# Kernel tuning notes

Measured on AMD Instinct MI355X. Metric: run time of the kernel, lower is better.

Reference implementation:

```python
import jax, jax.numpy as jnp
import numpy as np

N, E, H = 25000, 100000, 32          # nodes, edges, node/clique hidden dim
NC, A, EC = 8000, 50000, 24000       # cliques, node2clique assignments, clique edges
EEMB, CEE, L = 8, 8, 2               # edge emb dims, n layers


def segment_mean(vals, ids, num):
    s = jax.ops.segment_sum(vals, ids, num_segments=num)
    cnt = jax.ops.segment_sum(jnp.ones(ids.shape[0], vals.dtype), ids, num_segments=num)
    return s / jnp.maximum(cnt, 1.0)[:, None]


def setup_inputs() -> dict:
    key = jax.random.key(0)
    ks = jax.random.split(key, 24)
    s = 0.1  # param scale
    inp = {
        "node_features": jax.random.normal(ks[0], (N, H), jnp.float32),
        "edge_index": jax.random.randint(ks[1], (2, E), 0, N),
        "edge_features": jax.random.normal(ks[2], (E, EEMB), jnp.float32),
        "clique_features": jax.random.normal(ks[3], (NC, H), jnp.float32),
        "node2clique_index": jnp.stack([
            jax.random.randint(ks[4], (A,), 0, N),
            jax.random.randint(ks[5], (A,), 0, NC)]),
        "clique_edge_index": jax.random.randint(ks[6], (2, EC), 0, NC),
        "clique_edge_features": jax.random.normal(ks[7], (EC, CEE), jnp.float32),
        # node NNConv params (stacked over L layers)
        "nn1_w": jax.random.normal(ks[8], (L, EEMB, H)) * s,
        "nn1_b": jnp.zeros((L, H)),
        "nn2_w": jax.random.normal(ks[9], (L, H, H * H)) * s,
        "nn2_b": jnp.zeros((L, H * H)),
        "root_w": jax.random.normal(ks[10], (L, H, H)) * s,
        "root_b": jnp.zeros((L, H)),
        # Node2Clique linear
        "n2c_w": jax.random.normal(ks[11], (L, H, H)) * s,
        "n2c_b": jnp.zeros((L, H)),
        # clique NNConv params
        "cnn1_w": jax.random.normal(ks[12], (L, CEE, H)) * s,
        "cnn1_b": jnp.zeros((L, H)),
        "cnn2_w": jax.random.normal(ks[13], (L, H, H * H)) * s,
        "cnn2_b": jnp.zeros((L, H * H)),
        "croot_w": jax.random.normal(ks[14], (L, H, H)) * s,
        "croot_b": jnp.zeros((L, H)),
        # Clique2Node linear
        "c2n_w": jax.random.normal(ks[15], (L, H, H)) * s,
        "c2n_b": jnp.zeros((L, H)),
    }
    return inp


def nnconv(x, src, dst, edge_attr, w1, b1, w2, b2, rw, rb, n_out_nodes):
    # per-edge weight matrices from the edge MLP: [E, in, out]
    h = jax.nn.relu(edge_attr @ w1 + b1)
    We = (h @ w2 + b2).reshape(edge_attr.shape[0], x.shape[1], -1)
    msg = jnp.einsum('ei,eio->eo', x[src], We)           # message from source
    agg = segment_mean(msg, dst, n_out_nodes)            # mean aggregation at target
    return agg + x @ rw + rb                             # root weight + bias


def reference(node_features, edge_index, edge_features, clique_features,
              node2clique_index, clique_edge_index, clique_edge_features,
              nn1_w, nn1_b, nn2_w, nn2_b, root_w, root_b, n2c_w, n2c_b,
              cnn1_w, cnn1_b, cnn2_w, cnn2_b, croot_w, croot_b, c2n_w, c2n_b):
    x, c = node_features, clique_features
    src, dst = edge_index[0], edge_index[1]
    nid, cid = node2clique_index[0], node2clique_index[1]
    csrc, cdst = clique_edge_index[0], clique_edge_index[1]
    for l in range(L):
        # node-level edge-conditioned conv
        x = jax.nn.relu(nnconv(x, src, dst, edge_features,
                               nn1_w[l], nn1_b[l], nn2_w[l], nn2_b[l],
                               root_w[l], root_b[l], N))
        # Node2Clique: project node feats, scatter-mean into cliques
        m = x @ n2c_w[l] + n2c_b[l]
        c = c + segment_mean(m[nid], cid, NC)
        # clique-level edge-conditioned conv
        c = jax.nn.relu(nnconv(c, csrc, cdst, clique_edge_features,
                               cnn1_w[l], cnn1_b[l], cnn2_w[l], cnn2_b[l],
                               croot_w[l], croot_b[l], NC))
        # Clique2Node: project clique feats, scatter-mean back onto nodes
        m = c @ c2n_w[l] + c2n_b[l]
        x = x + segment_mean(m[cid], nid, N)
    return (x, c)
```

## Files before the change

kernel.cpp:

```cpp
#include <hip/hip_runtime.h>
#include <hip/hip_bf16.h>

typedef unsigned int u32;
typedef unsigned short u16;

#define DEVINL __device__ __forceinline__

constexpr int Nn  = 25000;
constexpr int Ee  = 100000;
constexpr int NCc = 8000;
constexpr int Aa  = 50000;
constexpr int ECc = 24000;
constexpr int TCOLS = 1088;
constexpr int WPSZ  = TCOLS*32;
constexpr int TT_ROW = 561;
constexpr int NB_N = (Nn + 255)/256;
constexpr int NB_C = (NCc + 255)/256;
constexpr int PB_EN = (Ee + 255)/256;
constexpr int PB_EC = (ECc + 255)/256;
constexpr int PB_AS = (2*Aa + 255)/256;
constexpr int PB_WP = (4*WPSZ + 255)/256;

typedef float f32x4 __attribute__((ext_vector_type(4)));
typedef _Float16 h16x2 __attribute__((ext_vector_type(2)));
typedef _Float16 h16x8 __attribute__((ext_vector_type(8)));

DEVINL float b2f(u16 u){ union{u32 i;float f;}v; v.i = ((u32)u)<<16; return v.f; }
DEVINL float bfl(u32 u){ union{u32 i;float f;}v; v.i = u<<16; return v.f; }
DEVINL float bfh(u32 u){ union{u32 i;float f;}v; v.i = u & 0xffff0000u; return v.f; }
DEVINL u16 f2b(float f){ union{float f;u32 i;}v; v.f=f; u32 i=v.i;
  return (u16)((i + 0x7fffu + ((i>>16)&1u)) >> 16); }
DEVINL u16 f2h(float x){ union{ _Float16 h; u16 u; } v; v.h = (_Float16)x; return v.u; }
DEVINL u32 pkh2(float a, float b){
  union{ _Float16 h[2]; u32 u; } v;
  v.h[0] = (_Float16)a; v.h[1] = (_Float16)b; return v.u;
}
DEVINL float ldw(const void* p, long i, int f){
  return f ? ((const float*)p)[i] : b2f(((const u16*)p)[i]);
}
DEVINL float dot2f(u32 a, u32 b, float c){
  union U{u32 u; h16x2 h;};
  U ua; ua.u = a; U ub; ub.u = b;
#if __has_builtin(__builtin_amdgcn_fdot2)
  return __builtin_amdgcn_fdot2(ua.h, ub.h, c, false);
#else
  return c + (float)ua.h[0]*(float)ub.h[0] + (float)ua.h[1]*(float)ub.h[1];
#endif
}

__global__ __launch_bounds__(256) void k_detect_count(const u16* __restrict__ p, int n,
                        u32* __restrict__ maxbits, int* __restrict__ zcnt,
                        int* __restrict__ done, int* __restrict__ flag,
                        const int* __restrict__ ei, const int* __restrict__ cei,
                        const int* __restrict__ n2c,
                        int* __restrict__ deg_nd, int* __restrict__ deg_ce,
                        int* __restrict__ deg_n2c, int* __restrict__ deg_c2n,
                        int* __restrict__ cnt_sn, int* __restrict__ cnt_sc){
  int i0 = blockIdx.x*256 + threadIdx.x;
  { int t = i0;
    if (t < Ee)                             atomicAdd(&deg_nd[ei[Ee + t]], 1);
    else if ((t -= Ee) < ECc)               atomicAdd(&deg_ce[cei[ECc + t]], 1);
    else if ((t -= ECc) < Aa)               atomicAdd(&deg_n2c[n2c[Aa + t]], 1);
    else if ((t -= Aa) < Aa)                atomicAdd(&deg_c2n[n2c[t]], 1);
    else if ((t -= Aa) < Ee)                atomicAdd(&cnt_sn[ei[t]], 1);
    else if ((t -= Ee) < ECc)               atomicAdd(&cnt_sc[cei[t]], 1);
  }
  if (blockIdx.x >= 256) return;
  float lm = 0.f; int lz = 0;
  for (int i = i0; i < n; i += 256*256){
    u16 v = p[i];
    if (v == 0) lz++;
    lm = fmaxf(lm, fabsf(b2f(v)));
  }
  #pragma unroll
  for (int off = 32; off; off >>= 1){
    lm = fmaxf(lm, __shfl_down(lm, off));
    lz += __shfl_down(lz, off);
  }
  __shared__ float smax[4]; __shared__ int szc[4];
  if ((threadIdx.x & 63) == 0){
    smax[threadIdx.x >> 6] = lm;
    szc[threadIdx.x >> 6] = lz;
  }
  __syncthreads();
  if (threadIdx.x == 0){
    float m = fmaxf(fmaxf(smax[0], smax[1]), fmaxf(smax[2], smax[3]));
    int z = szc[0] + szc[1] + szc[2] + szc[3];
    atomicMax(maxbits, __float_as_uint(m));
    atomicAdd(zcnt, z);
    __threadfence();
    if (atomicAdd(done, 1) == 255){
      float mm = __uint_as_float(*maxbits);
      *flag = (mm > 1e6f || *zcnt > n/4) ? 1 : 0;
    }
  }
}

__global__ __launch_bounds__(256) void k_scan_block(
    const int* __restrict__ c0, const int* __restrict__ c1,
    const int* __restrict__ c2, const int* __restrict__ c3,
    int* __restrict__ o0, int* __restrict__ o1, int* __restrict__ o2, int* __restrict__ o3,
    int* __restrict__ b0, int* __restrict__ b1, int* __restrict__ b2, int* __restrict__ b3){
  __shared__ int s[256];
  int bid = blockIdx.x, seg, rb;
  if (bid < NB_N){ seg=0; rb=bid; }
  else if (bid < NB_N+NB_C){ seg=1; rb=bid-NB_N; }
  else if (bid < 2*NB_N+NB_C){ seg=2; rb=bid-NB_N-NB_C; }
  else { seg=3; rb=bid-2*NB_N-NB_C; }
  const int* cnt = seg==0?c0 : seg==1?c1 : seg==2?c2 : c3;
  int* offs = seg==0?o0 : seg==1?o1 : seg==2?o2 : o3;
  int* bs   = seg==0?b0 : seg==1?b1 : seg==2?b2 : b3;
  int M = (seg & 1) ? NCc : Nn;
  int tid = threadIdx.x;
  int i = rb*256 + tid;
  int v = (i < M) ? cnt[i] : 0;
  s[tid] = v; __syncthreads();
  for (int d = 1; d < 256; d <<= 1){
    int t = (tid >= d) ? s[tid-d] : 0;
    __syncthreads();
    s[tid] += t;
    __syncthreads();
  }
  if (i < M) offs[i] = s[tid] - v;
  if (tid == 255) bs[rb] = s[255];
}

__global__ __launch_bounds__(256) void k_scan_fix2(
    int* __restrict__ o0, int* __restrict__ o1, int* __restrict__ o2, int* __restrict__ o3,
    const int* __restrict__ b0, const int* __restrict__ b1,
    const int* __restrict__ b2, const int* __restrict__ b3){
  __shared__ int s[256];
  int bid = blockIdx.x, seg, rb;
  if (bid < NB_N){ seg=0; rb=bid; }
  else if (bid < NB_N+NB_C){ seg=1; rb=bid-NB_N; }
  else if (bid < 2*NB_N+NB_C){ seg=2; rb=bid-NB_N-NB_C; }
  else { seg=3; rb=bid-2*NB_N-NB_C; }
  int* offs = seg==0?o0 : seg==1?o1 : seg==2?o2 : o3;
  const int* bsp = seg==0?b0 : seg==1?b1 : seg==2?b2 : b3;
  int M = (seg & 1) ? NCc : Nn;
  int tid = threadIdx.x;
  int v = (tid < rb) ? bsp[tid] : 0;
  s[tid] = v; __syncthreads();
  #pragma unroll
  for (int d = 128; d; d >>= 1){
    if (tid < d) s[tid] += s[tid + d];
    __syncthreads();
  }
  int prefix = s[0];
  int i = rb*256 + tid;
  if (i < M) offs[i] += prefix;
}

__global__ __launch_bounds__(256) void k_place_pack(
    const int* __restrict__ ei, const int* __restrict__ cei, const int* __restrict__ n2c,
    const void* __restrict__ ef, const void* __restrict__ cef,
    const void* __restrict__ nn1w, const void* __restrict__ nn1b,
    const void* __restrict__ cnn1w, const void* __restrict__ cnn1b,
    const void* __restrict__ nn2w, const void* __restrict__ nn2b, const void* __restrict__ rootw,
    const void* __restrict__ cnn2w, const void* __restrict__ cnn2b, const void* __restrict__ crootw,
    const int* __restrict__ offs_n, const int* __restrict__ offs_c,
    const int* __restrict__ offs_an, const int* __restrict__ offs_ac,
    int* __restrict__ cur_n, int* __restrict__ cur_c,
    int* __restrict__ cur_an, int* __restrict__ cur_ac,
    int2* __restrict__ sdp_n, int2* __restrict__ sdp_c,
    u32* __restrict__ hp_n, u32* __restrict__ hp_c,
    int* __restrict__ an2c, int* __restrict__ ac2n,
    const int* __restrict__ flag, u16* __restrict__ Wp4){
  int b = blockIdx.x, tid = threadIdx.x;
  int f = *flag;
  if (b < PB_EN + PB_EC){
    __shared__ float w1s[2][256], b1s[2][32];
    int isC = (b >= PB_EN);
    int e = (isC ? b - PB_EN : b)*256 + tid;
    int E = isC ? ECc : Ee;
    const void* W1 = isC ? cnn1w : nn1w;
    const void* B1 = isC ? cnn1b : nn1b;
    w1s[0][tid] = ldw(W1, tid, f);
    w1s[1][tid] = ldw(W1, 256 + tid, f);
    if (tid < 32){ b1s[0][tid] = ldw(B1, tid, f); b1s[1][tid] = ldw(B1, 32 + tid, f); }
    __syncthreads();
    if (e < E){
      const int* EI = isC ? cei : ei;
      int s = EI[e], d = EI[E + e];
      int* cur = isC ? cur_c : cur_n;
      const int* offs = isC ? offs_c : offs_n;
      int p = offs[s] + atomicAdd(&cur[s], 1);
      (isC ? sdp_c : sdp_n)[p] = make_int2(s, d);
      const void* EF = isC ? cef : ef;
      float ev[8];
      #pragma unroll
      for (int j = 0; j < 8; j++) ev[j] = ldw(EF, (long)e*8 + j, f);
      u32* hp = isC ? hp_c : hp_n;
      #pragma unroll
      for (int l = 0; l < 2; l++){
        u32* hq = hp + (size_t)l*E*16 + (size_t)p*16;
        #pragma unroll
        for (int kk = 0; kk < 16; kk++){
          float a0 = b1s[l][2*kk], a1 = b1s[l][2*kk+1];
          #pragma unroll
          for (int j = 0; j < 8; j++){
            a0 += ev[j]*w1s[l][j*32 + 2*kk];
            a1 += ev[j]*w1s[l][j*32 + 2*kk + 1];
          }
          hq[kk] = pkh2(fmaxf(a0, 0.f), fmaxf(a1, 0.f));
        }
      }
    }
  } else if (b < PB_EN + PB_EC + PB_AS){
    int i = (b - PB_EN - PB_EC)*256 + tid;
    if (i < Aa){
      int c = n2c[Aa + i];
      an2c[offs_ac[c] + atomicAdd(&cur_ac[c], 1)] = n2c[i];
    } else if ((i -= Aa) < Aa){
      int nd = n2c[i];
      ac2n[offs_an[nd] + atomicAdd(&cur_an[nd], 1)] = n2c[Aa + i];
    }
  } else {
    int i = (b - PB_EN - PB_EC - PB_AS)*256 + tid;
    if (i >= 4*WPSZ) return;
    int set = i / WPSZ, j = i - set*WPSZ;
    int l = set >> 1, isC = set & 1;
    const void* W2 = isC ? cnn2w : nn2w;
    const void* B2 = isC ? cnn2b : nn2b;
    const void* RW = isC ? crootw : rootw;
    int col = j >> 5, ii = j & 31;
    float v;
    if (col < 1024)      v = ldw(W2, (long)l*32768 + ((col>>5)<<10) + (ii<<5) + (col&31), f);
    else if (col < 1056) v = ldw(B2, (long)l*1024 + (ii<<5) + (col-1024), f);
    else                 v = ldw(RW, (long)l*1024 + (ii<<5) + (col-1056), f);
    Wp4[i] = f2h(v);
  }
}

__global__ __launch_bounds__(512) void k_conv_fused(const void* __restrict__ base, int braw,
                           const float* __restrict__ addagg, const int* __restrict__ adddeg, int M,
                           const int2* __restrict__ sdp, const u32* __restrict__ hp,
                           const int* __restrict__ offs, int E_,
                           const u16* __restrict__ Wp,
                           const void* __restrict__ rb, long rboff,
                           const int* __restrict__ flag,
                           float* __restrict__ feat_root, float* __restrict__ agg){
  __shared__ __align__(16) u32 Tt[16*TT_ROW];
  __shared__ u32 hws[8][64];
  int tid = threadIdx.x;
  int w = tid >> 6, lane = tid & 63;
  int quad = lane >> 4, lm = lane & 15;
  int n0 = blockIdx.x * 16;
  int f = *flag;
  int n = n0 + lm;
  int nc = n < M ? n : M-1;
  long bidx = (long)nc*32 + quad*8;
  float fv[8];
  if (braw && f == 0){
    uint4 q = *(const uint4*)((const u16*)base + bidx);
    fv[0]=bfl(q.x); fv[1]=bfh(q.x); fv[2]=bfl(q.y); fv[3]=bfh(q.y);
    fv[4]=bfl(q.z); fv[5]=bfh(q.z); fv[6]=bfl(q.w); fv[7]=bfh(q.w);
  } else {
    const float4* bp = (const float4*)((const float*)base + bidx);
    float4 q0 = bp[0], q1 = bp[1];
    fv[0]=q0.x; fv[1]=q0.y; fv[2]=q0.z; fv[3]=q0.w;
    fv[4]=q1.x; fv[5]=q1.y; fv[6]=q1.z; fv[7]=q1.w;
  }
  if (addagg){
    int dg = adddeg[nc];
    float d = (float)(dg > 1 ? dg : 1);
    const float4* ap = (const float4*)(addagg + (size_t)nc*32 + quad*8);
    float4 a0 = ap[0], a1 = ap[1];
    float inv = 1.f/d;
    fv[0]+=a0.x*inv; fv[1]+=a0.y*inv; fv[2]+=a0.z*inv; fv[3]+=a0.w*inv;
    fv[4]+=a1.x*inv; fv[5]+=a1.y*inv; fv[6]+=a1.z*inv; fv[7]+=a1.w*inv;
  }
  union { h16x8 v; u32 u[4]; } bf;
  #pragma unroll
  for (int j = 0; j < 4; j++) bf.u[j] = pkh2(fv[2*j], fv[2*j+1]);

  #define AFR(ct) (*(const h16x8*)(Wp + (size_t)((ct)*16 + lm)*32 + quad*8))
  f32x4 z4 = {0.f, 0.f, 0.f, 0.f};
  #pragma unroll
  for (int g = 0; g < 2; g++){
    int q = w + 8*g;
    f32x4 c0 = __builtin_amdgcn_mfma_f32_16x16x32_f16(AFR(4*q+0), bf.v, z4, 0, 0, 0);
    f32x4 c1 = __builtin_amdgcn_mfma_f32_16x16x32_f16(AFR(4*q+1), bf.v, z4, 0, 0, 0);
    f32x4 c2 = __builtin_amdgcn_mfma_f32_16x16x32_f16(AFR(4*q+2), bf.v, z4, 0, 0, 0);
    f32x4 c3 = __builtin_amdgcn_mfma_f32_16x16x32_f16(AFR(4*q+3), bf.v, z4, 0, 0, 0);
    int rbase = lm*TT_ROW;
    int ob = quad*4;
    #pragma unroll
    for (int i = 0; i < 4; i++){
      Tt[rbase + (ob+i)*17 + q]      = pkh2(c0[i], c2[i]);
      Tt[rbase + (16+ob+i)*17 + q]   = pkh2(c1[i], c3[i]);
    }
  }
  if (w < 4){
    int ct = 64 + w;
    f32x4 c = __builtin_amdgcn_mfma_f32_16x16x32_f16(AFR(ct), bf.v, z4, 0, 0, 0);
    if (ct < 66){
      int p0 = (ct-64)*8 + quad*2;
      Tt[lm*TT_ROW + 544 + p0]     = pkh2(c[0], c[1]);
      Tt[lm*TT_ROW + 544 + p0 + 1] = pkh2(c[2], c[3]);
    } else if (n < M){
      int o = (ct-66)*16 + quad*4;
      float4 v = make_float4(c[0] + ldw(rb, rboff+o,   f),
                             c[1] + ldw(rb, rboff+o+1, f),
                             c[2] + ldw(rb, rboff+o+2, f),
                             c[3] + ldw(rb, rboff+o+3, f));
      *(float4*)&feat_root[(size_t)n*32 + o] = v;
    }
  }
  __syncthreads();

  int lo = offs[n0];
  int hi = (n0 + 16 < M) ? offs[n0 + 16] : E_;
  int eg = quad, kk = lm;
  int pos = lo + w*4;
  u32 hp0 = 0, hp1 = 0; int sd0 = 0, sd1 = 0;
  { int idx = pos*16 + lane;      if (idx < hi*16) hp0 = hp[idx];
    idx = (pos+32)*16 + lane;     if (idx < hi*16) hp1 = hp[idx]; }
  if (lane < 8){
    int idx = pos*2 + lane;       if (idx < hi*2) sd0 = ((const int*)sdp)[idx];
    idx = (pos+32)*2 + lane;      if (idx < hi*2) sd1 = ((const int*)sdp)[idx];
  }
  for (; pos < hi; pos += 32){
    int np = pos + 64;
    u32 hp2 = 0; int sd2 = 0;
    { int idx = np*16 + lane; if (idx < hi*16) hp2 = hp[idx]; }
    if (lane < 8){ int idx = np*2 + lane; if (idx < hi*2) sd2 = ((const int*)sdp)[idx]; }
    hws[w][lane] = hp0;
    int sn = __shfl(sd0, 2*eg);
    int dn = __shfl(sd0, 2*eg + 1);
    bool valid = (pos + eg < hi);
    int sr = sn - n0; sr = sr < 0 ? 0 : (sr > 15 ? 15 : sr);
    const u32* Tr = Tt + sr*TT_ROW;
    const u32* T0 = Tr + 34*kk;
    const u32* Hp = &hws[w][eg*16];
    union{u32 u; h16x2 h;} b2u; b2u.u = Tr[544 + kk];
    float m0 = (float)b2u.h[0], m1 = (float)b2u.h[1];
    #pragma unroll
    for (int kq = 0; kq < 16; kq++){
      u32 hv = Hp[kq];
      u32 t0 = T0[kq];
      u32 t1 = T0[17 + kq];
      m0 = dot2f(hv, t0, m0);
      m1 = dot2f(hv, t1, m1);
    }
    if (valid){
      float* ap = agg + (size_t)dn*32 + 2*kk;
      atomicAdd(ap,   m0);
      atomicAdd(ap+1, m1);
    }
    hp0 = hp1; sd0 = sd1; hp1 = hp2; sd1 = sd2;
  }
  #undef AFR
}

__global__ __launch_bounds__(256) void k_update_lin(const float* __restrict__ agg, const int* __restrict__ deg,
                           const float* __restrict__ feat_root, int M,
                           const void* __restrict__ w, long woff,
                           const void* __restrict__ b, long boff,
                           const int* __restrict__ flag,
                           float* __restrict__ feat,
                           const int* __restrict__ sidx, const int* __restrict__ soffs,
                           const int* __restrict__ sdeg, float* __restrict__ sagg){
  __shared__ float wsm[1024], bs[32], rows[8][33];
  int tid = threadIdx.x;
  int f = *flag;
  for (int idx = tid; idx < 1024; idx += 256) wsm[idx] = ldw(w, woff + idx, f);
  if (tid < 32) bs[tid] = ldw(b, boff + tid, f);
  int nl = tid >> 5, o = tid & 31;
  int n = blockIdx.x*8 + nl;
  long i = (long)n*32 + o;
  if (n < M){
    int dg = deg[n];
    float d = (float)(dg > 1 ? dg : 1);
    float v = fmaxf(agg[i]/d + feat_root[i], 0.f);
    rows[nl][o] = v;
    feat[i] = v;
  }
  __syncthreads();
  if (n >= M) return;
  float acc = bs[o];
  #pragma unroll
  for (int j = 0; j < 32; j++) acc += rows[nl][j]*wsm[j*32+o];
  int slo = soffs[n], scnt = sdeg[n];
  for (int a = 0; a < scnt; a++)
    atomicAdd(&sagg[(size_t)sidx[slo + a]*32 + o], acc);
}

__global__ __launch_bounds__(256) void k_store(const float* __restrict__ x, const float* __restrict__ xagg,
                      const int* __restrict__ xdeg, const float* __restrict__ c,
                      void* __restrict__ out, const int* __restrict__ flag){
  int i = blockIdx.x*256 + threadIdx.x;
  int tot = Nn*32 + NCc*32;
  if (i >= tot) return;
  float v;
  if (i < Nn*32){
    int n = i >> 5;
    int dg = xdeg[n];
    float d = (float)(dg > 1 ? dg : 1);
    v = x[i] + xagg[i]/d;
  } else v = c[i - Nn*32];
  if (*flag) ((float*)out)[i] = v;
  else       ((u16*)out)[i]   = f2b(v);
}

extern "C" void kernel_launch(void* const* d_in, const int* in_sizes, int n_in,
                              void* d_out, int out_size, void* d_ws, size_t ws_size,
                              hipStream_t stream){
  const int* ei  = (const int*)d_in[1];
  const int* n2c = (const int*)d_in[4];
  const int* cei = (const int*)d_in[5];
  const void *efr = d_in[2], *cefr = d_in[6];
  const void *nn1w = d_in[7], *nn1b = d_in[8], *nn2w = d_in[9], *nn2b = d_in[10],
             *rootw = d_in[11], *rootb = d_in[12], *n2cw = d_in[13], *n2cb = d_in[14],
             *cnn1w = d_in[15], *cnn1b = d_in[16], *cnn2w = d_in[17], *cnn2b = d_in[18],
             *crootw = d_in[19], *crootb = d_in[20], *c2nw = d_in[21], *c2nb = d_in[22];

  char* ws = (char*)d_ws;
  size_t off = 0;
  auto alloc = [&](size_t bytes){ void* p = ws + off; off += (bytes + 255) & ~(size_t)255; return p; };

  size_t zstart = off;
  float* aggE0  = (float*)alloc((size_t)Nn*32*4);
  float* aggE1  = (float*)alloc((size_t)Nn*32*4);
  float* caggE0 = (float*)alloc((size_t)NCc*32*4);
  float* caggE1 = (float*)alloc((size_t)NCc*32*4);
  float* caggS0 = (float*)alloc((size_t)NCc*32*4);
  float* caggS1 = (float*)alloc((size_t)NCc*32*4);
  float* aggS0  = (float*)alloc((size_t)Nn*32*4);
  float* aggS1  = (float*)alloc((size_t)Nn*32*4);
  int* deg_nd  = (int*)alloc((size_t)Nn*4);
  int* deg_ce  = (int*)alloc((size_t)NCc*4);
  int* deg_n2c = (int*)alloc((size_t)NCc*4);
  int* deg_c2n = (int*)alloc((size_t)Nn*4);
  int* cnt_sn  = (int*)alloc((size_t)Nn*4);
  int* cnt_sc  = (int*)alloc((size_t)NCc*4);
  int* cur_n   = (int*)alloc((size_t)Nn*4);
  int* cur_c   = (int*)alloc((size_t)NCc*4);
  int* cur_an  = (int*)alloc((size_t)Nn*4);
  int* cur_ac  = (int*)alloc((size_t)NCc*4);
  u32* maxbits = (u32*)alloc(256);
  int* zcnt = (int*)((char*)maxbits + 4);
  int* flag = (int*)((char*)maxbits + 8);
  int* done = (int*)((char*)maxbits + 12);
  size_t zbytes = off - zstart;

  float* xB  = (float*)alloc((size_t)Nn*32*4);
  float* xC  = (float*)alloc((size_t)Nn*32*4);
  float* cC0 = (float*)alloc((size_t)NCc*32*4);
  float* cC1 = (float*)alloc((size_t)NCc*32*4);
  float* frn = (float*)alloc((size_t)Nn*32*4);
  float* frc = (float*)alloc((size_t)NCc*32*4);
  int* offs_n  = (int*)alloc((size_t)Nn*4);
  int* offs_c  = (int*)alloc((size_t)NCc*4);
  int* offs_an = (int*)alloc((size_t)Nn*4);
  int* offs_ac = (int*)alloc((size_t)NCc*4);
  int* bs0 = (int*)alloc(512); int* bs1 = (int*)alloc(512);
  int* bs2 = (int*)alloc(512); int* bs3 = (int*)alloc(512);
  int* an2c = (int*)alloc((size_t)Aa*4);
  int* ac2n = (int*)alloc((size_t)Aa*4);
  int2* sdp_n = (int2*)alloc((size_t)Ee*8);
  int2* sdp_c = (int2*)alloc((size_t)ECc*8);
  u16* Wp4 = (u16*)alloc((size_t)4*WPSZ*2);
  u32* hp_n = (u32*)alloc((size_t)2*Ee*16*4);
  u32* hp_c = (u32*)alloc((size_t)2*ECc*16*4);

  auto nb = [](int n){ return (n + 255)/256; };

  hipMemsetAsync(ws + zstart, 0, zbytes, stream);
  k_detect_count<<<nb(2*Ee + 2*ECc + 2*Aa),256,0,stream>>>((const u16*)d_in[0], Nn*32,
      maxbits, zcnt, done, flag, ei, cei, n2c,
      deg_nd, deg_ce, deg_n2c, deg_c2n, cnt_sn, cnt_sc);
  k_scan_block<<<2*(NB_N+NB_C),256,0,stream>>>(cnt_sn, cnt_sc, deg_c2n, deg_n2c,
      offs_n, offs_c, offs_an, offs_ac, bs0, bs1, bs2, bs3);
  k_scan_fix2<<<2*(NB_N+NB_C),256,0,stream>>>(offs_n, offs_c, offs_an, offs_ac,
      bs0, bs1, bs2, bs3);
  k_place_pack<<<PB_EN+PB_EC+PB_AS+PB_WP,256,0,stream>>>(ei, cei, n2c, efr, cefr,
      nn1w, nn1b, cnn1w, cnn1b, nn2w, nn2b, rootw, cnn2w, cnn2b, crootw,
      offs_n, offs_c, offs_an, offs_ac, cur_n, cur_c, cur_an, cur_ac,
      sdp_n, sdp_c, hp_n, hp_c, an2c, ac2n, flag, Wp4);

  int Gn = (Nn + 15)/16, Gc = (NCc + 15)/16;

  k_conv_fused<<<Gn,512,0,stream>>>(d_in[0], 1, nullptr, nullptr, Nn, sdp_n, hp_n, offs_n, Ee,
      Wp4 + 0*WPSZ, rootb, 0, flag, frn, aggE0);
  k_update_lin<<<(Nn+7)/8,256,0,stream>>>(aggE0, deg_nd, frn, Nn, n2cw, 0, n2cb, 0, flag,
      xB, ac2n, offs_an, deg_c2n, caggS0);
  k_conv_fused<<<Gc,512,0,stream>>>(d_in[3], 1, caggS0, deg_n2c, NCc, sdp_c, hp_c, offs_c, ECc,
      Wp4 + 1*WPSZ, crootb, 0, flag, frc, caggE0);
  k_update_lin<<<(NCc+7)/8,256,0,stream>>>(caggE0, deg_ce, frc, NCc, c2nw, 0, c2nb, 0, flag,
      cC0, an2c, offs_ac, deg_n2c, aggS0);
  k_conv_fused<<<Gn,512,0,stream>>>(xB, 0, aggS0, deg_c2n, Nn, sdp_n, hp_n + (size_t)Ee*16, offs_n, Ee,
      Wp4 + 2*WPSZ, rootb, 32, flag, frn, aggE1);
  k_update_lin<<<(Nn+7)/8,256,0,stream>>>(aggE1, deg_nd, frn, Nn, n2cw, 1024, n2cb, 32, flag,
      xC, ac2n, offs_an, deg_c2n, caggS1);
  k_conv_fused<<<Gc,512,0,stream>>>(cC0, 0, caggS1, deg_n2c, NCc, sdp_c, hp_c + (size_t)ECc*16, offs_c, ECc,
      Wp4 + 3*WPSZ, crootb, 32, flag, frc, caggE1);
  k_update_lin<<<(NCc+7)/8,256,0,stream>>>(caggE1, deg_ce, frc, NCc, c2nw, 1024, c2nb, 32, flag,
      cC1, an2c, offs_ac, deg_n2c, aggS1);
  k_store<<<nb(Nn*32 + NCc*32),256,0,stream>>>(xC, aggS1, deg_c2n, cC1, d_out, flag);
}
```

Before: 294.5 us.

## Replace atomic scatter aggregation with destination-sorted message slots and gather-sum

Float atomics are replaced everywhere. Each edge gets a slot in a destination-sorted (CSR) message buffer, the conv kernel writes per-edge messages with plain stores, and the update kernel sums them per destination. Node2clique and clique2node scatter-means become pull-style gathers in the next conv kernel and in the final store kernel. This removes atomic contention and the zeroing of the aggregation buffers, and makes summation order deterministic. The cost is an extra prefix scan over destination degrees, a large per-edge message buffer (E×32 floats) written and read back, and serial per-thread loops over variable degree.

```diff
diff --git a/kernel.cpp b/kernel.cpp
--- a/kernel.cpp
+++ b/kernel.cpp
@@ -96,20 +96,34 @@
   }
 }
 
-__global__ __launch_bounds__(256) void k_scan_block(
+DEVINL void segof(int bid, int& seg, int& rb){
+  seg = 0; rb = bid;
+  while (true){
+    int nb = (seg & 1) ? NB_C : NB_N;
+    if (rb < nb) break;
+    rb -= nb; seg++;
+  }
+}
+
+__global__ __launch_bounds__(256) void k_scan_block6(
     const int* __restrict__ c0, const int* __restrict__ c1,
     const int* __restrict__ c2, const int* __restrict__ c3,
-    int* __restrict__ o0, int* __restrict__ o1, int* __restrict__ o2, int* __restrict__ o3,
-    int* __restrict__ b0, int* __restrict__ b1, int* __restrict__ b2, int* __restrict__ b3){
+    const int* __restrict__ c4, const int* __restrict__ c5,
+    int* __restrict__ o0, int* __restrict__ o1, int* __restrict__ o2,
+    int* __restrict__ o3, int* __restrict__ o4, int* __restrict__ o5,
+    int* __restrict__ b0, int* __restrict__ b1, int* __restrict__ b2,
+    int* __restrict__ b3, int* __restrict__ b4, int* __restrict__ b5){
   __shared__ int s[256];
-  int bid = blockIdx.x, seg, rb;
-  if (bid < NB_N){ seg=0; rb=bid; }
-  else if (bid < NB_N+NB_C){ seg=1; rb=bid-NB_N; }
-  else if (bid < 2*NB_N+NB_C){ seg=2; rb=bid-NB_N-NB_C; }
-  else { seg=3; rb=bid-2*NB_N-NB_C; }
-  const int* cnt = seg==0?c0 : seg==1?c1 : seg==2?c2 : c3;
-  int* offs = seg==0?o0 : seg==1?o1 : seg==2?o2 : o3;
-  int* bs   = seg==0?b0 : seg==1?b1 : seg==2?b2 : b3;
+  int seg, rb; segof(blockIdx.x, seg, rb);
+  const int* cnt; int* offs; int* bs;
+  switch (seg){
+    case 0: cnt=c0; offs=o0; bs=b0; break;
+    case 1: cnt=c1; offs=o1; bs=b1; break;
+    case 2: cnt=c2; offs=o2; bs=b2; break;
+    case 3: cnt=c3; offs=o3; bs=b3; break;
+    case 4: cnt=c4; offs=o4; bs=b4; break;
+    default: cnt=c5; offs=o5; bs=b5; break;
+  }
   int M = (seg & 1) ? NCc : Nn;
   int tid = threadIdx.x;
   int i = rb*256 + tid;
@@ -125,18 +139,22 @@
   if (tid == 255) bs[rb] = s[255];
 }
 
-__global__ __launch_bounds__(256) void k_scan_fix2(
-    int* __restrict__ o0, int* __restrict__ o1, int* __restrict__ o2, int* __restrict__ o3,
-    const int* __restrict__ b0, const int* __restrict__ b1,
-    const int* __restrict__ b2, const int* __restrict__ b3){
+__global__ __launch_bounds__(256) void k_scan_fix6(
+    int* __restrict__ o0, int* __restrict__ o1, int* __restrict__ o2,
+    int* __restrict__ o3, int* __restrict__ o4, int* __restrict__ o5,
+    const int* __restrict__ b0, const int* __restrict__ b1, const int* __restrict__ b2,
+    const int* __restrict__ b3, const int* __restrict__ b4, const int* __restrict__ b5){
   __shared__ int s[256];
-  int bid = blockIdx.x, seg, rb;
-  if (bid < NB_N){ seg=0; rb=bid; }
-  else if (bid < NB_N+NB_C){ seg=1; rb=bid-NB_N; }
-  else if (bid < 2*NB_N+NB_C){ seg=2; rb=bid-NB_N-NB_C; }
-  else { seg=3; rb=bid-2*NB_N-NB_C; }
-  int* offs = seg==0?o0 : seg==1?o1 : seg==2?o2 : o3;
-  const int* bsp = seg==0?b0 : seg==1?b1 : seg==2?b2 : b3;
+  int seg, rb; segof(blockIdx.x, seg, rb);
+  int* offs; const int* bsp;
+  switch (seg){
+    case 0: offs=o0; bsp=b0; break;
+    case 1: offs=o1; bsp=b1; break;
+    case 2: offs=o2; bsp=b2; break;
+    case 3: offs=o3; bsp=b3; break;
+    case 4: offs=o4; bsp=b4; break;
+    default: offs=o5; bsp=b5; break;
+  }
   int M = (seg & 1) ? NCc : Nn;
   int tid = threadIdx.x;
   int v = (tid < rb) ? bsp[tid] : 0;
@@ -160,8 +178,10 @@
     const void* __restrict__ cnn2w, const void* __restrict__ cnn2b, const void* __restrict__ crootw,
     const int* __restrict__ offs_n, const int* __restrict__ offs_c,
     const int* __restrict__ offs_an, const int* __restrict__ offs_ac,
+    const int* __restrict__ doffs_n, const int* __restrict__ doffs_c,
     int* __restrict__ cur_n, int* __restrict__ cur_c,
     int* __restrict__ cur_an, int* __restrict__ cur_ac,
+    int* __restrict__ cur_dn, int* __restrict__ cur_dc,
     int2* __restrict__ sdp_n, int2* __restrict__ sdp_c,
     u32* __restrict__ hp_n, u32* __restrict__ hp_c,
     int* __restrict__ an2c, int* __restrict__ ac2n,
@@ -185,7 +205,10 @@
       int* cur = isC ? cur_c : cur_n;
       const int* offs = isC ? offs_c : offs_n;
       int p = offs[s] + atomicAdd(&cur[s], 1);
-      (isC ? sdp_c : sdp_n)[p] = make_int2(s, d);
+      const int* dofs = isC ? doffs_c : doffs_n;
+      int* curd = isC ? cur_dc : cur_dn;
+      int dsl = dofs[d] + atomicAdd(&curd[d], 1);
+      (isC ? sdp_c : sdp_n)[p] = make_int2(s, dsl);
       const void* EF = isC ? cef : ef;
       float ev[8];
       #pragma unroll
@@ -233,15 +256,16 @@
 }
 
 __global__ __launch_bounds__(512) void k_conv_fused(const void* __restrict__ base, int braw,
-                           const float* __restrict__ addagg, const int* __restrict__ adddeg, int M,
+                           const float* __restrict__ adm, const int* __restrict__ sidx,
+                           const int* __restrict__ soffs, const int* __restrict__ sdeg, int M,
                            const int2* __restrict__ sdp, const u32* __restrict__ hp,
                            const int* __restrict__ offs, int E_,
                            const u16* __restrict__ Wp,
                            const void* __restrict__ rb, long rboff,
                            const int* __restrict__ flag,
-                           float* __restrict__ feat_root, float* __restrict__ agg){
+                           float* __restrict__ feat_root, float* __restrict__ msg){
   __shared__ __align__(16) u32 Tt[16*TT_ROW];
-  __shared__ u32 hws[8][64];
+  __shared__ __align__(16) u32 hws[8][64];
   int tid = threadIdx.x;
   int w = tid >> 6, lane = tid & 63;
   int quad = lane >> 4, lm = lane & 15;
@@ -261,14 +285,18 @@
     fv[0]=q0.x; fv[1]=q0.y; fv[2]=q0.z; fv[3]=q0.w;
     fv[4]=q1.x; fv[5]=q1.y; fv[6]=q1.z; fv[7]=q1.w;
   }
-  if (addagg){
-    int dg = adddeg[nc];
-    float d = (float)(dg > 1 ? dg : 1);
-    const float4* ap = (const float4*)(addagg + (size_t)nc*32 + quad*8);
-    float4 a0 = ap[0], a1 = ap[1];
-    float inv = 1.f/d;
-    fv[0]+=a0.x*inv; fv[1]+=a0.y*inv; fv[2]+=a0.z*inv; fv[3]+=a0.w*inv;
-    fv[4]+=a1.x*inv; fv[5]+=a1.y*inv; fv[6]+=a1.z*inv; fv[7]+=a1.w*inv;
+  if (adm){
+    int slo = soffs[nc], scnt = sdeg[nc];
+    float ac[8] = {0,0,0,0,0,0,0,0};
+    for (int k = 0; k < scnt; k++){
+      const float4* mp = (const float4*)(adm + (size_t)sidx[slo + k]*32 + quad*8);
+      float4 a0 = mp[0], a1 = mp[1];
+      ac[0]+=a0.x; ac[1]+=a0.y; ac[2]+=a0.z; ac[3]+=a0.w;
+      ac[4]+=a1.x; ac[5]+=a1.y; ac[6]+=a1.z; ac[7]+=a1.w;
+    }
+    float inv = 1.f/(float)(scnt > 1 ? scnt : 1);
+    #pragma unroll
+    for (int j = 0; j < 8; j++) fv[j] += ac[j]*inv;
   }
   union { h16x8 v; u32 u[4]; } bf;
   #pragma unroll
@@ -327,40 +355,39 @@
     if (lane < 8){ int idx = np*2 + lane; if (idx < hi*2) sd2 = ((const int*)sdp)[idx]; }
     hws[w][lane] = hp0;
     int sn = __shfl(sd0, 2*eg);
-    int dn = __shfl(sd0, 2*eg + 1);
+    int ds = __shfl(sd0, 2*eg + 1);
     bool valid = (pos + eg < hi);
     int sr = sn - n0; sr = sr < 0 ? 0 : (sr > 15 ? 15 : sr);
     const u32* Tr = Tt + sr*TT_ROW;
     const u32* T0 = Tr + 34*kk;
-    const u32* Hp = &hws[w][eg*16];
+    const uint4* Hp4 = (const uint4*)&hws[w][eg*16];
     union{u32 u; h16x2 h;} b2u; b2u.u = Tr[544 + kk];
     float m0 = (float)b2u.h[0], m1 = (float)b2u.h[1];
     #pragma unroll
-    for (int kq = 0; kq < 16; kq++){
-      u32 hv = Hp[kq];
-      u32 t0 = T0[kq];
-      u32 t1 = T0[17 + kq];
-      m0 = dot2f(hv, t0, m0);
-      m1 = dot2f(hv, t1, m1);
+    for (int g = 0; g < 4; g++){
+      uint4 hv4 = Hp4[g];
+      m0 = dot2f(hv4.x, T0[4*g+0], m0);  m1 = dot2f(hv4.x, T0[17+4*g+0], m1);
+      m0 = dot2f(hv4.y, T0[4*g+1], m0);  m1 = dot2f(hv4.y, T0[17+4*g+1], m1);
+      m0 = dot2f(hv4.z, T0[4*g+2], m0);  m1 = dot2f(hv4.z, T0[17+4*g+2], m1);
+      m0 = dot2f(hv4.w, T0[4*g+3], m0);  m1 = dot2f(hv4.w, T0[17+4*g+3], m1);
     }
     if (valid){
-      float* ap = agg + (size_t)dn*32 + 2*kk;
-      atomicAdd(ap,   m0);
-      atomicAdd(ap+1, m1);
+      float* ap = msg + (size_t)ds*32 + 2*kk;
+      ap[0] = m0;
+      ap[1] = m1;
     }
     hp0 = hp1; sd0 = sd1; hp1 = hp2; sd1 = sd2;
   }
   #undef AFR
 }
 
-__global__ __launch_bounds__(256) void k_update_lin(const float* __restrict__ agg, const int* __restrict__ deg,
+__global__ __launch_bounds__(256) void k_update_lin(const float* __restrict__ msg,
+                           const int* __restrict__ doffs, const int* __restrict__ deg,
                            const float* __restrict__ feat_root, int M,
                            const void* __restrict__ w, long woff,
                            const void* __restrict__ b, long boff,
                            const int* __restrict__ flag,
-                           float* __restrict__ feat,
-                           const int* __restrict__ sidx, const int* __restrict__ soffs,
-                           const int* __restrict__ sdeg, float* __restrict__ sagg){
+                           float* __restrict__ feat, float* __restrict__ mout){
   __shared__ float wsm[1024], bs[32], rows[8][33];
   int tid = threadIdx.x;
   int f = *flag;
@@ -370,9 +397,11 @@
   int n = blockIdx.x*8 + nl;
   long i = (long)n*32 + o;
   if (n < M){
-    int dg = deg[n];
+    int lo = doffs[n], dg = deg[n];
+    float a = 0.f;
+    for (int k = 0; k < dg; k++) a += msg[(size_t)(lo + k)*32 + o];
     float d = (float)(dg > 1 ? dg : 1);
-    float v = fmaxf(agg[i]/d + feat_root[i], 0.f);
+    float v = fmaxf(a/d + feat_root[i], 0.f);
     rows[nl][o] = v;
     feat[i] = v;
   }
@@ -381,23 +410,24 @@
   float acc = bs[o];
   #pragma unroll
   for (int j = 0; j < 32; j++) acc += rows[nl][j]*wsm[j*32+o];
-  int slo = soffs[n], scnt = sdeg[n];
-  for (int a = 0; a < scnt; a++)
-    atomicAdd(&sagg[(size_t)sidx[slo + a]*32 + o], acc);
-}
-
-__global__ __launch_bounds__(256) void k_store(const float* __restrict__ x, const float* __restrict__ xagg,
-                      const int* __restrict__ xdeg, const float* __restrict__ c,
+  mout[i] = acc;
+}
+
+__global__ __launch_bounds__(256) void k_store(const float* __restrict__ x,
+                      const float* __restrict__ mC, const int* __restrict__ sidx,
+                      const int* __restrict__ soffs, const int* __restrict__ sdeg,
+                      const float* __restrict__ c,
                       void* __restrict__ out, const int* __restrict__ flag){
   int i = blockIdx.x*256 + threadIdx.x;
   int tot = Nn*32 + NCc*32;
   if (i >= tot) return;
   float v;
   if (i < Nn*32){
-    int n = i >> 5;
-    int dg = xdeg[n];
-    float d = (float)(dg > 1 ? dg : 1);
-    v = x[i] + xagg[i]/d;
+    int n = i >> 5, o = i & 31;
+    int lo = soffs[n], dg = sdeg[n];
+    float a = 0.f;
+    for (int k = 0; k < dg; k++) a += mC[(size_t)sidx[lo + k]*32 + o];
+    v = x[i] + a/(float)(dg > 1 ? dg : 1);
   } else v = c[i - Nn*32];
   if (*flag) ((float*)out)[i] = v;
   else       ((u16*)out)[i]   = f2b(v);
@@ -420,14 +450,6 @@
   auto alloc = [&](size_t bytes){ void* p = ws + off; off += (bytes + 255) & ~(size_t)255; return p; };
 
   size_t zstart = off;
-  float* aggE0  = (float*)alloc((size_t)Nn*32*4);
-  float* aggE1  = (float*)alloc((size_t)Nn*32*4);
-  float* caggE0 = (float*)alloc((size_t)NCc*32*4);
-  float* caggE1 = (float*)alloc((size_t)NCc*32*4);
-  float* caggS0 = (float*)alloc((size_t)NCc*32*4);
-  float* caggS1 = (float*)alloc((size_t)NCc*32*4);
-  float* aggS0  = (float*)alloc((size_t)Nn*32*4);
-  float* aggS1  = (float*)alloc((size_t)Nn*32*4);
   int* deg_nd  = (int*)alloc((size_t)Nn*4);
   int* deg_ce  = (int*)alloc((size_t)NCc*4);
   int* deg_n2c = (int*)alloc((size_t)NCc*4);
@@ -438,6 +460,8 @@
   int* cur_c   = (int*)alloc((size_t)NCc*4);
   int* cur_an  = (int*)alloc((size_t)Nn*4);
   int* cur_ac  = (int*)alloc((size_t)NCc*4);
+  int* cur_dn  = (int*)alloc((size_t)Nn*4);
+  int* cur_dc  = (int*)alloc((size_t)NCc*4);
   u32* maxbits = (u32*)alloc(256);
   int* zcnt = (int*)((char*)maxbits + 4);
   int* flag = (int*)((char*)maxbits + 8);
@@ -450,12 +474,19 @@
   float* cC1 = (float*)alloc((size_t)NCc*32*4);
   float* frn = (float*)alloc((size_t)Nn*32*4);
   float* frc = (float*)alloc((size_t)NCc*32*4);
+  float* msgN = (float*)alloc((size_t)Ee*32*4);
+  float* msgC = (float*)alloc((size_t)ECc*32*4);
+  float* mN  = (float*)alloc((size_t)Nn*32*4);
+  float* mC  = (float*)alloc((size_t)NCc*32*4);
   int* offs_n  = (int*)alloc((size_t)Nn*4);
   int* offs_c  = (int*)alloc((size_t)NCc*4);
   int* offs_an = (int*)alloc((size_t)Nn*4);
   int* offs_ac = (int*)alloc((size_t)NCc*4);
+  int* doffs_n = (int*)alloc((size_t)Nn*4);
+  int* doffs_c = (int*)alloc((size_t)NCc*4);
   int* bs0 = (int*)alloc(512); int* bs1 = (int*)alloc(512);
   int* bs2 = (int*)alloc(512); int* bs3 = (int*)alloc(512);
+  int* bs4 = (int*)alloc(512); int* bs5 = (int*)alloc(512);
   int* an2c = (int*)alloc((size_t)Aa*4);
   int* ac2n = (int*)alloc((size_t)Aa*4);
   int2* sdp_n = (int2*)alloc((size_t)Ee*8);
@@ -470,32 +501,34 @@
   k_detect_count<<<nb(2*Ee + 2*ECc + 2*Aa),256,0,stream>>>((const u16*)d_in[0], Nn*32,
       maxbits, zcnt, done, flag, ei, cei, n2c,
       deg_nd, deg_ce, deg_n2c, deg_c2n, cnt_sn, cnt_sc);
-  k_scan_block<<<2*(NB_N+NB_C),256,0,stream>>>(cnt_sn, cnt_sc, deg_c2n, deg_n2c,
-      offs_n, offs_c, offs_an, offs_ac, bs0, bs1, bs2, bs3);
-  k_scan_fix2<<<2*(NB_N+NB_C),256,0,stream>>>(offs_n, offs_c, offs_an, offs_ac,
-      bs0, bs1, bs2, bs3);
+  k_scan_block6<<<3*(NB_N+NB_C),256,0,stream>>>(cnt_sn, cnt_sc, deg_c2n, deg_n2c, deg_nd, deg_ce,
+      offs_n, offs_c, offs_an, offs_ac, doffs_n, doffs_c,
+      bs0, bs1, bs2, bs3, bs4, bs5);
+  k_scan_fix6<<<3*(NB_N+NB_C),256,0,stream>>>(offs_n, offs_c, offs_an, offs_ac, doffs_n, doffs_c,
+      bs0, bs1, bs2, bs3, bs4, bs5);
   k_place_pack<<<PB_EN+PB_EC+PB_AS+PB_WP,256,0,stream>>>(ei, cei, n2c, efr, cefr,
       nn1w, nn1b, cnn1w, cnn1b, nn2w, nn2b, rootw, cnn2w, cnn2b, crootw,
-      offs_n, offs_c, offs_an, offs_ac, cur_n, cur_c, cur_an, cur_ac,
+      offs_n, offs_c, offs_an, offs_ac, doffs_n, doffs_c,
+      cur_n, cur_c, cur_an, cur_ac, cur_dn, cur_dc,
       sdp_n, sdp_c, hp_n, hp_c, an2c, ac2n, flag, Wp4);
 
   int Gn = (Nn + 15)/16, Gc = (NCc + 15)/16;
 
-  k_conv_fused<<<Gn,512,0,stream>>>(d_in[0], 1, nullptr, nullptr, Nn, sdp_n, hp_n, offs_n, Ee,
-      Wp4 + 0*WPSZ, rootb, 0, flag, frn, aggE0);
-  k_update_lin<<<(Nn+7)/8,256,0,stream>>>(aggE0, deg_nd, frn, Nn, n2cw, 0, n2cb, 0, flag,
-      xB, ac2n, offs_an, deg_c2n, caggS0);
-  k_conv_fused<<<Gc,512,0,stream>>>(d_in[3], 1, caggS0, deg_n2c, NCc, sdp_c, hp_c, offs_c, ECc,
-      Wp4 + 1*WPSZ, crootb, 0, flag, frc, caggE0);
-  k_update_lin<<<(NCc+7)/8,256,0,stream>>>(caggE0, deg_ce, frc, NCc, c2nw, 0, c2nb, 0, flag,
-      cC0, an2c, offs_ac, deg_n2c, aggS0);
-  k_conv_fused<<<Gn,512,0,stream>>>(xB, 0, aggS0, deg_c2n, Nn, sdp_n, hp_n + (size_t)Ee*16, offs_n, Ee,
-      Wp4 + 2*WPSZ, rootb, 32, flag, frn, aggE1);
-  k_update_lin<<<(Nn+7)/8,256,0,stream>>>(aggE1, deg_nd, frn, Nn, n2cw, 1024, n2cb, 32, flag,
-      xC, ac2n, offs_an, deg_c2n, caggS1);
-  k_conv_fused<<<Gc,512,0,stream>>>(cC0, 0, caggS1, deg_n2c, NCc, sdp_c, hp_c + (size_t)ECc*16, offs_c, ECc,
-      Wp4 + 3*WPSZ, crootb, 32, flag, frc, caggE1);
-  k_update_lin<<<(NCc+7)/8,256,0,stream>>>(caggE1, deg_ce, frc, NCc, c2nw, 1024, c2nb, 32, flag,
-      cC1, an2c, offs_ac, deg_n2c, aggS1);
-  k_store<<<nb(Nn*32 + NCc*32),256,0,stream>>>(xC, aggS1, deg_c2n, cC1, d_out, flag);
-}
+  k_conv_fused<<<Gn,512,0,stream>>>(d_in[0], 1, nullptr, nullptr, nullptr, nullptr, Nn,
+      sdp_n, hp_n, offs_n, Ee, Wp4 + 0*WPSZ, rootb, 0, flag, frn, msgN);
+  k_update_lin<<<(Nn+7)/8,256,0,stream>>>(msgN, doffs_n, deg_nd, frn, Nn,
+      n2cw, 0, n2cb, 0, flag, xB, mN);
+  k_conv_fused<<<Gc,512,0,stream>>>(d_in[3], 1, mN, an2c, offs_ac, deg_n2c, NCc,
+      sdp_c, hp_c, offs_c, ECc, Wp4 + 1*WPSZ, crootb, 0, flag, frc, msgC);
+  k_update_lin<<<(NCc+7)/8,256,0,stream>>>(msgC, doffs_c, deg_ce, frc, NCc,
+      c2nw, 0, c2nb, 0, flag, cC0, mC);
+  k_conv_fused<<<Gn,512,0,stream>>>(xB, 0, mC, ac2n, offs_an, deg_c2n, Nn,
+      sdp_n, hp_n + (size_t)Ee*16, offs_n, Ee, Wp4 + 2*WPSZ, rootb, 32, flag, frn, msgN);
+  k_update_lin<<<(Nn+7)/8,256,0,stream>>>(msgN, doffs_n, deg_nd, frn, Nn,
+      n2cw, 1024, n2cb, 32, flag, xC, mN);
+  k_conv_fused<<<Gc,512,0,stream>>>(cC0, 0, mN, an2c, offs_ac, deg_n2c, NCc,
+      sdp_c, hp_c + (size_t)ECc*16, offs_c, ECc, Wp4 + 3*WPSZ, crootb, 32, flag, frc, msgC);
+  k_update_lin<<<(NCc+7)/8,256,0,stream>>>(msgC, doffs_c, deg_ce, frc, NCc,
+      c2nw, 1024, c2nb, 32, flag, cC1, mC);
+  k_store<<<nb(Nn*32 + NCc*32),256,0,stream>>>(xC, mC, ac2n, offs_an, deg_c2n, cC1, d_out, flag);
+}
```

Result: no change. 289.3 us (-1.8%).
